# Performance work log

Measured on AMD Instinct MI355X. Metric: run time of the kernel, lower is better.

The kernel has to match this reference:

```python
import jax, jax.numpy as jnp
import numpy as np

BATCH = 1024
INPUT_DIM = 4096
HV_DIM = 8192          # == 2**NUM_QUBITS, so encode_classical fully overwrites the state
NUM_QUBITS = 13
QUANTUM_DEPTH = 3


def setup_inputs() -> dict:
    key = jax.random.key(0)
    k1, k2, k3 = jax.random.split(key, 3)
    x = jax.random.normal(k1, (BATCH, INPUT_DIM), dtype=jnp.float32)
    # torch nn.Linear weight layout: [out_features, in_features]
    W = jax.random.normal(k2, (HV_DIM, INPUT_DIM), dtype=jnp.float32)
    quantum_params = jax.random.normal(k3, (QUANTUM_DEPTH, NUM_QUBITS), dtype=jnp.float32)
    return {"x": x, "W": W, "quantum_params": quantum_params}


def reference(x, W, quantum_params):
    # projection: classical_hv = x @ W^T  -> [B, HV_DIM]
    classical = x @ W.T
    # encode_classical: normalize, cast to complex, renormalize (second norm is 1;
    # kept for fidelity with the original code path)
    amps = (classical / jnp.linalg.norm(classical, axis=-1, keepdims=True)).astype(jnp.complex64)
    amps = amps / jnp.linalg.norm(amps, axis=-1, keepdims=True)

    # sequential gate sequence: for depth in range(D): for qubit in range(Q):
    #   amps = amps*cos(a/2) + roll(amps, 1)*sin(a/2)*1j
    # each step uses the updated amplitudes -> lax.scan over the flattened angles
    angles = quantum_params.reshape(-1)  # [D*Q], depth-major matching the loop order

    def step(a, angle):
        c = jnp.cos(angle * 0.5)
        s = jnp.sin(angle * 0.5)
        return a * c + jnp.roll(a, 1, axis=-1) * (s * 1j), None

    amps, _ = jax.lax.scan(step, amps, angles)
    return amps  # [B, 2**NUM_QUBITS] complex64 quantum amplitudes
```

## Files before the change

### kernel.cpp

```cpp
#include <hip/hip_runtime.h>
#include <hip/hip_fp16.h>
#include <math.h>

typedef _Float16 half8 __attribute__((ext_vector_type(8)));
typedef __fp16 fp16x2 __attribute__((ext_vector_type(2)));
typedef float f32x4 __attribute__((ext_vector_type(4)));

#define BATCH 1024
#define IN_DIM 4096
#define HV 8192
#define NTAP 40

#define BM 128
#define BN 128
#define BK 32
#define BKP 36

#define BM2 128
#define BN2 256
#define BK2 64
#define NT2 (IN_DIM / BK2)
#define ASZ (BM2 * BK2)
#define BSZ (BN2 * BK2)
#define TSZ (ASZ + BSZ)

#define GLD16(g, l) __builtin_amdgcn_global_load_lds(                          \
    (const __attribute__((address_space(1))) void*)(g),                        \
    (__attribute__((address_space(3))) void*)(l), 16, 0, 0)

static __device__ __forceinline__ half8 pk8(f32x4 a, f32x4 b) {
    union { fp16x2 p[4]; half8 h; } u;
    u.p[0] = __builtin_amdgcn_cvt_pkrtz(a.x, a.y);
    u.p[1] = __builtin_amdgcn_cvt_pkrtz(a.z, a.w);
    u.p[2] = __builtin_amdgcn_cvt_pkrtz(b.x, b.y);
    u.p[3] = __builtin_amdgcn_cvt_pkrtz(b.z, b.w);
    return u.h;
}

typedef _Float16 half4v __attribute__((ext_vector_type(4)));
__global__ __launch_bounds__(256) void cvt_f32_f16(const float4* __restrict__ src,
                                                   half4v* __restrict__ dst, int n4) {
    int i = blockIdx.x * 256 + threadIdx.x;
    if (i < n4) {
        float4 v = src[i];
        half4v h;
        h.x = (_Float16)v.x; h.y = (_Float16)v.y;
        h.z = (_Float16)v.z; h.w = (_Float16)v.w;
        dst[i] = h;
    }
}

__global__ __launch_bounds__(64) void compute_taps(const float* __restrict__ qp,
                                                   float* __restrict__ taps) {
    const int lane = threadIdx.x;
    float qv = (lane < 39) ? qp[lane] : 0.f;
    float pr = (lane == 0) ? 1.f : 0.f;
    float pim = 0.f;
    for (int t = 0; t < 39; t++) {
        float a = __shfl(qv, t, 64) * 0.5f;
        float c = cosf(a), s = sinf(a);
        float ur = __shfl_up(pr, 1, 64);
        float ui = __shfl_up(pim, 1, 64);
        if (lane == 0) { ur = 0.f; ui = 0.f; }
        float nr = c * pr - s * ui;
        float ni = c * pim + s * ur;
        pr = nr; pim = ni;
    }
    if (lane < NTAP) taps[lane] = pr;
}

__global__ __launch_bounds__(512, 2) void gemm_f16(
        const _Float16* __restrict__ A,
        const _Float16* __restrict__ B,
        float* __restrict__ out,
        long out_n) {
    __shared__ __align__(16) _Float16 lds[3 * TSZ];

    const int tid  = threadIdx.x;
    const int lane = tid & 63;
    const int wave = tid >> 6;
    const int wm = wave & 1;
    const int wn = wave >> 1;
    const int q = lane >> 4, r = lane & 15;
    const int bm = blockIdx.y * BM2;
    const int bn = blockIdx.x * BN2;

    const _Float16* srcA[2];
    int dA[2];
    #pragma unroll
    for (int h = 0; h < 2; h++) {
        const int p = h * 512 + tid;
        const int R = p >> 3, c = (p & 7) ^ (R & 7);
        srcA[h] = A + (size_t)(bm + R) * IN_DIM + c * 8;
        dA[h] = (h * 512 + wave * 64) * 8;
    }
    const _Float16* srcB[4];
    int dB[4];
    #pragma unroll
    for (int h = 0; h < 4; h++) {
        const int p = h * 512 + tid;
        const int R = p >> 3, c = (p & 7) ^ (R & 7);
        srcB[h] = B + (size_t)(bn + R) * IN_DIM + c * 8;
        dB[h] = ASZ + (h * 512 + wave * 64) * 8;
    }

    f32x4 acc[4][4] = {};

#define STAGE(u, k0)  do {                                   \
        _Float16* bp = &lds[(u) * TSZ];                      \
        GLD16(srcA[0] + (k0), bp + dA[0]);                   \
        GLD16(srcA[1] + (k0), bp + dA[1]);                   \
        GLD16(srcB[0] + (k0), bp + dB[0]);                   \
        GLD16(srcB[1] + (k0), bp + dB[1]);                   \
        GLD16(srcB[2] + (k0), bp + dB[2]);                   \
        GLD16(srcB[3] + (k0), bp + dB[3]);                   \
    } while (0)

#define COMPUTE(u)  do {                                                            \
        const _Float16* bp = &lds[(u) * TSZ];                                       \
        half8 af[4][2], bf[4][2];                                                   \
        _Pragma("unroll")                                                           \
        for (int i = 0; i < 4; i++)                                                 \
            _Pragma("unroll")                                                       \
            for (int kk = 0; kk < 2; kk++) {                                        \
                const int R = wm * 64 + i * 16 + r;                                 \
                const int sw = (kk * 4 + q) ^ (r & 7);                              \
                af[i][kk] = *(const half8*)&bp[R * 64 + sw * 8];                    \
            }                                                                       \
        _Pragma("unroll")                                                           \
        for (int j = 0; j < 4; j++)                                                 \
            _Pragma("unroll")                                                       \
            for (int kk = 0; kk < 2; kk++) {                                        \
                const int R = wn * 64 + j * 16 + r;                                 \
                const int sw = (kk * 4 + q) ^ (r & 7);                              \
                bf[j][kk] = *(const half8*)&bp[ASZ + R * 64 + sw * 8];              \
            }                                                                       \
        __builtin_amdgcn_s_setprio(1);                                              \
        _Pragma("unroll")                                                           \
        for (int i = 0; i < 4; i++)                                                 \
            _Pragma("unroll")                                                       \
            for (int j = 0; j < 4; j++)                                             \
                _Pragma("unroll")                                                   \
                for (int kk = 0; kk < 2; kk++)                                      \
                    acc[i][j] = __builtin_amdgcn_mfma_f32_16x16x32_f16(             \
                        af[i][kk], bf[j][kk], acc[i][j], 0, 0, 0);                  \
        __builtin_amdgcn_s_setprio(0);                                              \
    } while (0)

    STAGE(0, 0);
    STAGE(1, BK2);
    int cur = 0;
    for (int t = 0; t < NT2 - 1; ++t) {
        asm volatile("s_waitcnt vmcnt(6)" ::: "memory");
        __builtin_amdgcn_sched_barrier(0);
        __builtin_amdgcn_s_barrier();
        if (t + 2 < NT2) {
            const int nxt = (cur + 2 >= 3) ? cur - 1 : cur + 2;
            STAGE(nxt, (t + 2) * BK2);
        }
        COMPUTE(cur);
        cur = (cur + 1 == 3) ? 0 : cur + 1;
    }
    asm volatile("s_waitcnt vmcnt(0)" ::: "memory");
    __builtin_amdgcn_sched_barrier(0);
    __builtin_amdgcn_s_barrier();
    COMPUTE(cur);
#undef STAGE
#undef COMPUTE

    #pragma unroll
    for (int i = 0; i < 4; i++) {
        const int row = bm + wm * 64 + i * 16 + q * 4;
        #pragma unroll
        for (int j = 0; j < 4; j++) {
            const int col = bn + wn * 64 + j * 16 + r;
            #pragma unroll
            for (int reg = 0; reg < 4; reg++) {
                long idx = (long)(row + reg) * HV + col;
                if (idx < out_n) out[idx] = acc[i][j][reg];
            }
        }
    }
}

__global__ __launch_bounds__(256) void gemm_f32in(
        const float* __restrict__ A, const float* __restrict__ B,
        float* __restrict__ out, long out_n) {
    __shared__ __align__(16) float lgA[BM * BKP];
    __shared__ __align__(16) float lgB[BN * BKP];

    const int tid  = threadIdx.x;
    const int lane = tid & 63;
    const int wave = tid >> 6;
    const int wm = wave & 1, wn = wave >> 1;
    const int q = lane >> 4, r = lane & 15;
    const int bm = blockIdx.y * BM;
    const int bn = blockIdx.x * BN;

    const int rg = lane >> 3;
    const int cg = (lane & 7) * 4;
    const float* gA = A + (size_t)(bm + wave * 32 + rg) * IN_DIM + cg;
    const float* gB = B + (size_t)(bn + wave * 32 + rg) * IN_DIM + cg;
    float* lA = &lgA[(wave * 32 + rg) * BKP + cg];
    float* lB = &lgB[(wave * 32 + rg) * BKP + cg];

    f32x4 acc[4][4] = {};

    for (int k0 = 0; k0 < IN_DIM; k0 += BK) {
        float4 va[4], vb[4];
        #pragma unroll
        for (int i = 0; i < 4; i++) {
            va[i] = *(const float4*)(gA + k0 + (size_t)(8 * i) * IN_DIM);
            vb[i] = *(const float4*)(gB + k0 + (size_t)(8 * i) * IN_DIM);
        }
        __syncthreads();
        #pragma unroll
        for (int i = 0; i < 4; i++) {
            *(float4*)(lA + 8 * i * BKP) = va[i];
            *(float4*)(lB + 8 * i * BKP) = vb[i];
        }
        __syncthreads();

        half8 af[4], bf[4];
        #pragma unroll
        for (int i = 0; i < 4; i++) {
            const float* p = &lgA[(wm * 64 + i * 16 + r) * BKP + q * 8];
            af[i] = pk8(*(const f32x4*)p, *(const f32x4*)(p + 4));
        }
        #pragma unroll
        for (int j = 0; j < 4; j++) {
            const float* p = &lgB[(wn * 64 + j * 16 + r) * BKP + q * 8];
            bf[j] = pk8(*(const f32x4*)p, *(const f32x4*)(p + 4));
        }

        #pragma unroll
        for (int i = 0; i < 4; i++)
            #pragma unroll
            for (int j = 0; j < 4; j++)
                acc[i][j] = __builtin_amdgcn_mfma_f32_16x16x32_f16(af[i], bf[j], acc[i][j], 0, 0, 0);
    }

    #pragma unroll
    for (int i = 0; i < 4; i++) {
        const int row = bm + wm * 64 + i * 16 + q * 4;
        #pragma unroll
        for (int j = 0; j < 4; j++) {
            const int col = bn + wn * 64 + j * 16 + r;
            #pragma unroll
            for (int reg = 0; reg < 4; reg++) {
                long idx = (long)(row + reg) * HV + col;
                if (idx < out_n) out[idx] = acc[i][j][reg];
            }
        }
    }
}

#define SW4(p4) ((p4) ^ (((p4) >> 3) & 7))
#define WEL(u) (((u) & 3) == 0 ? w4[(u) >> 2].x : ((u) & 3) == 1 ? w4[(u) >> 2].y : \
                ((u) & 3) == 2 ? w4[(u) >> 2].z : w4[(u) >> 2].w)
__global__ __launch_bounds__(256, 2) void norm_conv(float* __restrict__ out,
                                                    const float* __restrict__ qp,
                                                    const float* __restrict__ taps,
                                                    long out_n) {
    __shared__ __align__(16) float ldsv[40 + HV + 24];
    __shared__ float scr[NTAP];
    __shared__ float red[4];

    const int b = blockIdx.x;
    if ((long)(b + 1) * HV > out_n) return;

    const int tid = threadIdx.x;
    const int lane = tid & 63;
    const int wave = tid >> 6;
    float* rowp = out + (size_t)b * HV;
    const float4* row4 = (const float4*)rowp;
    float4* l4 = (float4*)ldsv;

    float ss = 0.f;
    #pragma unroll
    for (int it = 0; it < 8; it++) {
        int j = it * 256 + tid;
        float4 v = row4[j];
        ss += v.x * v.x + v.y * v.y + v.z * v.z + v.w * v.w;
        l4[SW4(10 + j)] = v;
    }
    if (tid < NTAP) {
        ldsv[(SW4(tid >> 2) << 2) | (tid & 3)] = rowp[HV - NTAP + tid];
    }

    #pragma unroll
    for (int off = 32; off > 0; off >>= 1) ss += __shfl_down(ss, off, 64);
    if (lane == 0) red[wave] = ss;

    if (taps) {
        if (tid < NTAP) scr[tid] = taps[tid];
    } else if (wave == 0) {
        float qv = (lane < 39) ? qp[lane] : 0.f;
        float pr = (lane == 0) ? 1.f : 0.f;
        float pim = 0.f;
        for (int t = 0; t < 39; t++) {
            float a = __shfl(qv, t, 64) * 0.5f;
            float c = cosf(a), s = sinf(a);
            float ur = __shfl_up(pr, 1, 64);
            float ui = __shfl_up(pim, 1, 64);
            if (lane == 0) { ur = 0.f; ui = 0.f; }
            float nr = c * pr - s * ui;
            float ni = c * pim + s * ur;
            pr = nr; pim = ni;
        }
        if (lane < NTAP) scr[lane] = pr;
    }
    __syncthreads();

    const float inv = 1.0f / sqrtf(red[0] + red[1] + red[2] + red[3]);
    float4* out4 = (float4*)rowp;

    #pragma unroll
    for (int g = 0; g < 4; g++) {
        float4 w4[12];
        #pragma unroll
        for (int t = 0; t < 12; t++) w4[t] = l4[SW4(8 * tid + 2 * g + t)];

        float av[8] = {};
        #pragma unroll
        for (int k = 0; k < NTAP; k++) {
            const float c = scr[k];
            #pragma unroll
            for (int o = 0; o < 8; o++) av[o] += c * WEL(40 + o - k);
        }
        const int f4 = 8 * tid + 2 * g;
        out4[f4]     = make_float4(inv * av[0], inv * av[1], inv * av[2], inv * av[3]);
        out4[f4 + 1] = make_float4(inv * av[4], inv * av[5], inv * av[6], inv * av[7]);
    }
}

extern "C" void kernel_launch(void* const* d_in, const int* in_sizes, int n_in,
                              void* d_out, int out_size, void* d_ws, size_t ws_size,
                              hipStream_t stream) {
    const float* x  = (const float*)d_in[0];
    const float* W  = (const float*)d_in[1];
    const float* qp = (const float*)d_in[2];
    float* out = (float*)d_out;
    long out_n = (long)out_size;

    const size_t need = (size_t)BATCH * IN_DIM * 2 + (size_t)HV * IN_DIM * 2;

    if (ws_size >= need) {
        _Float16* xh = (_Float16*)d_ws;
        _Float16* wh = xh + (size_t)BATCH * IN_DIM;
        float* taps = nullptr;
        if (ws_size >= need + 256) {
            taps = (float*)((char*)d_ws + need);
            compute_taps<<<1, 64, 0, stream>>>(qp, taps);
        }
        int n4x = BATCH * IN_DIM / 4;
        int n4w = HV * IN_DIM / 4;
        cvt_f32_f16<<<n4x / 256, 256, 0, stream>>>((const float4*)x, (half4v*)xh, n4x);
        cvt_f32_f16<<<n4w / 256, 256, 0, stream>>>((const float4*)W, (half4v*)wh, n4w);
        dim3 grid2(HV / BN2, BATCH / BM2);
        gemm_f16<<<grid2, 512, 0, stream>>>(xh, wh, out, out_n);
        norm_conv<<<BATCH, 256, 0, stream>>>(out, qp, taps, out_n);
    } else {
        float* taps = nullptr;
        if (ws_size >= 256) {
            taps = (float*)d_ws;
            compute_taps<<<1, 64, 0, stream>>>(qp, taps);
        }
        dim3 grid(HV / BN, BATCH / BM);
        gemm_f32in<<<grid, 256, 0, stream>>>(x, W, out, out_n);
        norm_conv<<<BATCH, 256, 0, stream>>>(out, qp, taps, out_n);
    }
}
```

Before: 307.9 us.

## Fuse W fp32-to-fp16 conversion into GEMM and merge tap computation into prep

Removes the separate pass that converts W (32M floats) to fp16. The GEMM now loads fp32 W tiles into registers, converts them and writes them to LDS. The pipeline changes from a three-stage DMA ring to a double buffer that overlaps the next A DMA and B register loads with compute. The tap computation is folded into the x-conversion kernel as an extra block, which saves a launch. The cost is that W is read at fp32 width by every M-tile block (8 of them) instead of once, register pressure goes up, and the pipeline is shallower.

```diff
diff --git a/kernel.cpp b/kernel.cpp
--- a/kernel.cpp
+++ b/kernel.cpp
@@ -38,8 +38,11 @@
 }
 
 typedef _Float16 half4v __attribute__((ext_vector_type(4)));
-__global__ __launch_bounds__(256) void cvt_f32_f16(const float4* __restrict__ src,
-                                                   half4v* __restrict__ dst, int n4) {
+
+__global__ __launch_bounds__(256) void prep(const float4* __restrict__ src,
+                                            half4v* __restrict__ dst, int n4,
+                                            const float* __restrict__ qp,
+                                            float* __restrict__ taps) {
     int i = blockIdx.x * 256 + threadIdx.x;
     if (i < n4) {
         float4 v = src[i];
@@ -47,34 +50,31 @@
         h.x = (_Float16)v.x; h.y = (_Float16)v.y;
         h.z = (_Float16)v.z; h.w = (_Float16)v.w;
         dst[i] = h;
-    }
-}
-
-__global__ __launch_bounds__(64) void compute_taps(const float* __restrict__ qp,
-                                                   float* __restrict__ taps) {
-    const int lane = threadIdx.x;
-    float qv = (lane < 39) ? qp[lane] : 0.f;
-    float pr = (lane == 0) ? 1.f : 0.f;
-    float pim = 0.f;
-    for (int t = 0; t < 39; t++) {
-        float a = __shfl(qv, t, 64) * 0.5f;
-        float c = cosf(a), s = sinf(a);
-        float ur = __shfl_up(pr, 1, 64);
-        float ui = __shfl_up(pim, 1, 64);
-        if (lane == 0) { ur = 0.f; ui = 0.f; }
-        float nr = c * pr - s * ui;
-        float ni = c * pim + s * ur;
-        pr = nr; pim = ni;
-    }
-    if (lane < NTAP) taps[lane] = pr;
-}
-
-__global__ __launch_bounds__(512, 2) void gemm_f16(
+    } else if (blockIdx.x == (unsigned)(n4 / 256) && threadIdx.x < 64) {
+        const int lane = threadIdx.x;
+        float qv = (lane < 39) ? qp[lane] : 0.f;
+        float pr = (lane == 0) ? 1.f : 0.f;
+        float pim = 0.f;
+        for (int t = 0; t < 39; t++) {
+            float a = __shfl(qv, t, 64) * 0.5f;
+            float c = cosf(a), s = sinf(a);
+            float ur = __shfl_up(pr, 1, 64);
+            float ui = __shfl_up(pim, 1, 64);
+            if (lane == 0) { ur = 0.f; ui = 0.f; }
+            float nr = c * pr - s * ui;
+            float ni = c * pim + s * ur;
+            pr = nr; pim = ni;
+        }
+        if (lane < NTAP) taps[lane] = pr;
+    }
+}
+
+__global__ __launch_bounds__(512, 2) void gemm_fused(
         const _Float16* __restrict__ A,
-        const _Float16* __restrict__ B,
+        const float*    __restrict__ W,
         float* __restrict__ out,
         long out_n) {
-    __shared__ __align__(16) _Float16 lds[3 * TSZ];
+    __shared__ __align__(16) _Float16 lds[2 * TSZ];
 
     const int tid  = threadIdx.x;
     const int lane = tid & 63;
@@ -94,26 +94,45 @@
         srcA[h] = A + (size_t)(bm + R) * IN_DIM + c * 8;
         dA[h] = (h * 512 + wave * 64) * 8;
     }
-    const _Float16* srcB[4];
-    int dB[4];
+    const float* srcBW[4];
+    int dBo[4];
     #pragma unroll
     for (int h = 0; h < 4; h++) {
         const int p = h * 512 + tid;
         const int R = p >> 3, c = (p & 7) ^ (R & 7);
-        srcB[h] = B + (size_t)(bn + R) * IN_DIM + c * 8;
-        dB[h] = ASZ + (h * 512 + wave * 64) * 8;
+        srcBW[h] = W + (size_t)(bn + R) * IN_DIM + c * 8;
+        dBo[h] = ASZ + p * 8;
     }
 
     f32x4 acc[4][4] = {};
-
-#define STAGE(u, k0)  do {                                   \
-        _Float16* bp = &lds[(u) * TSZ];                      \
-        GLD16(srcA[0] + (k0), bp + dA[0]);                   \
-        GLD16(srcA[1] + (k0), bp + dA[1]);                   \
-        GLD16(srcB[0] + (k0), bp + dB[0]);                   \
-        GLD16(srcB[1] + (k0), bp + dB[1]);                   \
-        GLD16(srcB[2] + (k0), bp + dB[2]);                   \
-        GLD16(srcB[3] + (k0), bp + dB[3]);                   \
+    f32x4 brg[8];
+
+#define A_DMA(u, k0)  do {                                   \
+        _Float16* bpA = &lds[(u) * TSZ];                     \
+        GLD16(srcA[0] + (k0), bpA + dA[0]);                  \
+        GLD16(srcA[1] + (k0), bpA + dA[1]);                  \
+    } while (0)
+
+#define B_LOAD(k0)  do {                                     \
+        _Pragma("unroll")                                    \
+        for (int h = 0; h < 4; h++) {                        \
+            brg[2*h]   = *(const f32x4*)(srcBW[h] + (k0));   \
+            brg[2*h+1] = *(const f32x4*)(srcBW[h] + (k0) + 4); \
+        }                                                    \
+    } while (0)
+
+#define CVT_WRITE(u)  do {                                   \
+        _Float16* bpW = &lds[(u) * TSZ];                     \
+        _Pragma("unroll")                                    \
+        for (int h = 0; h < 4; h++) {                        \
+            f32x4 lo = brg[2*h], hi = brg[2*h+1];            \
+            half8 hv;                                        \
+            hv[0] = (_Float16)lo.x; hv[1] = (_Float16)lo.y;  \
+            hv[2] = (_Float16)lo.z; hv[3] = (_Float16)lo.w;  \
+            hv[4] = (_Float16)hi.x; hv[5] = (_Float16)hi.y;  \
+            hv[6] = (_Float16)hi.z; hv[7] = (_Float16)hi.w;  \
+            *(half8*)&bpW[dBo[h]] = hv;                      \
+        }                                                    \
     } while (0)
 
 #define COMPUTE(u)  do {                                                            \
@@ -147,25 +166,37 @@
         __builtin_amdgcn_s_setprio(0);                                              \
     } while (0)
 
-    STAGE(0, 0);
-    STAGE(1, BK2);
-    int cur = 0;
-    for (int t = 0; t < NT2 - 1; ++t) {
-        asm volatile("s_waitcnt vmcnt(6)" ::: "memory");
-        __builtin_amdgcn_sched_barrier(0);
-        __builtin_amdgcn_s_barrier();
-        if (t + 2 < NT2) {
-            const int nxt = (cur + 2 >= 3) ? cur - 1 : cur + 2;
-            STAGE(nxt, (t + 2) * BK2);
-        }
-        COMPUTE(cur);
-        cur = (cur + 1 == 3) ? 0 : cur + 1;
-    }
-    asm volatile("s_waitcnt vmcnt(0)" ::: "memory");
+    B_LOAD(0);
+    A_DMA(0, 0);
+    CVT_WRITE(0);
+    B_LOAD(BK2);
+    asm volatile("s_waitcnt vmcnt(8)" ::: "memory");
+    asm volatile("s_waitcnt lgkmcnt(0)" ::: "memory");
     __builtin_amdgcn_sched_barrier(0);
     __builtin_amdgcn_s_barrier();
-    COMPUTE(cur);
-#undef STAGE
+
+    int cur = 0;
+    for (int t = 0; t < NT2; ++t) {
+        const int nxt = cur ^ 1;
+        if (t + 1 < NT2) A_DMA(nxt, (t + 1) * BK2);
+        COMPUTE(cur);
+        if (t + 1 < NT2) {
+            CVT_WRITE(nxt);
+            if (t + 2 < NT2) {
+                B_LOAD((t + 2) * BK2);
+                asm volatile("s_waitcnt vmcnt(8)" ::: "memory");
+            } else {
+                asm volatile("s_waitcnt vmcnt(0)" ::: "memory");
+            }
+            asm volatile("s_waitcnt lgkmcnt(0)" ::: "memory");
+            __builtin_amdgcn_sched_barrier(0);
+            __builtin_amdgcn_s_barrier();
+        }
+        cur = nxt;
+    }
+#undef A_DMA
+#undef B_LOAD
+#undef CVT_WRITE
 #undef COMPUTE
 
     #pragma unroll
@@ -343,31 +374,19 @@
     float* out = (float*)d_out;
     long out_n = (long)out_size;
 
-    const size_t need = (size_t)BATCH * IN_DIM * 2 + (size_t)HV * IN_DIM * 2;
+    const size_t need = (size_t)BATCH * IN_DIM * 2 + 256;
 
     if (ws_size >= need) {
         _Float16* xh = (_Float16*)d_ws;
-        _Float16* wh = xh + (size_t)BATCH * IN_DIM;
-        float* taps = nullptr;
-        if (ws_size >= need + 256) {
-            taps = (float*)((char*)d_ws + need);
-            compute_taps<<<1, 64, 0, stream>>>(qp, taps);
-        }
+        float* taps = (float*)((char*)d_ws + (size_t)BATCH * IN_DIM * 2);
         int n4x = BATCH * IN_DIM / 4;
-        int n4w = HV * IN_DIM / 4;
-        cvt_f32_f16<<<n4x / 256, 256, 0, stream>>>((const float4*)x, (half4v*)xh, n4x);
-        cvt_f32_f16<<<n4w / 256, 256, 0, stream>>>((const float4*)W, (half4v*)wh, n4w);
+        prep<<<n4x / 256 + 1, 256, 0, stream>>>((const float4*)x, (half4v*)xh, n4x, qp, taps);
         dim3 grid2(HV / BN2, BATCH / BM2);
-        gemm_f16<<<grid2, 512, 0, stream>>>(xh, wh, out, out_n);
+        gemm_fused<<<grid2, 512, 0, stream>>>(xh, W, out, out_n);
         norm_conv<<<BATCH, 256, 0, stream>>>(out, qp, taps, out_n);
     } else {
-        float* taps = nullptr;
-        if (ws_size >= 256) {
-            taps = (float*)d_ws;
-            compute_taps<<<1, 64, 0, stream>>>(qp, taps);
-        }
         dim3 grid(HV / BN, BATCH / BM);
         gemm_f32in<<<grid, 256, 0, stream>>>(x, W, out, out_n);
-        norm_conv<<<BATCH, 256, 0, stream>>>(out, qp, taps, out_n);
-    }
-}
+        norm_conv<<<BATCH, 256, 0, stream>>>(out, qp, nullptr, out_n);
+    }
+}
```

After: 318.3 us. +3.4%, slower.

## Shrink f16 GEMM tile to 128x128x32 and fuse conversion and tap kernels

Applied to the files above, without the earlier changes.

The f16 GEMM goes from 128x256 tiles with BK=64 and 512 threads to 128x128 tiles with BK=32 and 256 threads. The LDS swizzle and the wait counts are adjusted to match, and the smaller LDS footprint per block should allow more resident blocks and a larger grid. The separate x/W f32-to-f16 conversions and the tap computation are merged into one prep kernel to remove launches. The cost is smaller per-block reuse and twice as many k-iterations, each with a barrier.

```diff
diff --git a/kernel.cpp b/kernel.cpp
--- a/kernel.cpp
+++ b/kernel.cpp
@@ -13,16 +13,12 @@
 
 #define BM 128
 #define BN 128
-#define BK 32
 #define BKP 36
 
-#define BM2 128
-#define BN2 256
-#define BK2 64
-#define NT2 (IN_DIM / BK2)
-#define ASZ (BM2 * BK2)
-#define BSZ (BN2 * BK2)
-#define TSZ (ASZ + BSZ)
+#define BK3 32
+#define NT3 (IN_DIM / BK3)
+#define ASZ3 (BM * BK3)
+#define TSZ3 (2 * ASZ3)
 
 #define GLD16(g, l) __builtin_amdgcn_global_load_lds(                          \
     (const __attribute__((address_space(1))) void*)(g),                        \
@@ -38,43 +34,52 @@
 }
 
 typedef _Float16 half4v __attribute__((ext_vector_type(4)));
-__global__ __launch_bounds__(256) void cvt_f32_f16(const float4* __restrict__ src,
-                                                   half4v* __restrict__ dst, int n4) {
-    int i = blockIdx.x * 256 + threadIdx.x;
-    if (i < n4) {
-        float4 v = src[i];
+
+__global__ __launch_bounds__(256) void prep(const float4* __restrict__ xsrc, int n4x,
+                                            const float4* __restrict__ wsrc, int n4w,
+                                            half4v* __restrict__ xdst,
+                                            half4v* __restrict__ wdst,
+                                            const float* __restrict__ qp,
+                                            float* __restrict__ taps) {
+    long i = (long)blockIdx.x * 256 + threadIdx.x;
+    if (i < n4x) {
+        float4 v = xsrc[i];
         half4v h;
         h.x = (_Float16)v.x; h.y = (_Float16)v.y;
         h.z = (_Float16)v.z; h.w = (_Float16)v.w;
-        dst[i] = h;
-    }
-}
-
-__global__ __launch_bounds__(64) void compute_taps(const float* __restrict__ qp,
-                                                   float* __restrict__ taps) {
-    const int lane = threadIdx.x;
-    float qv = (lane < 39) ? qp[lane] : 0.f;
-    float pr = (lane == 0) ? 1.f : 0.f;
-    float pim = 0.f;
-    for (int t = 0; t < 39; t++) {
-        float a = __shfl(qv, t, 64) * 0.5f;
-        float c = cosf(a), s = sinf(a);
-        float ur = __shfl_up(pr, 1, 64);
-        float ui = __shfl_up(pim, 1, 64);
-        if (lane == 0) { ur = 0.f; ui = 0.f; }
-        float nr = c * pr - s * ui;
-        float ni = c * pim + s * ur;
-        pr = nr; pim = ni;
-    }
-    if (lane < NTAP) taps[lane] = pr;
-}
-
-__global__ __launch_bounds__(512, 2) void gemm_f16(
+        xdst[i] = h;
+    } else if (i < (long)n4x + n4w) {
+        long j = i - n4x;
+        float4 v = wsrc[j];
+        half4v h;
+        h.x = (_Float16)v.x; h.y = (_Float16)v.y;
+        h.z = (_Float16)v.z; h.w = (_Float16)v.w;
+        wdst[j] = h;
+    } else if (threadIdx.x < 64) {
+        const int lane = threadIdx.x;
+        float qv = (lane < 39) ? qp[lane] : 0.f;
+        float pr = (lane == 0) ? 1.f : 0.f;
+        float pim = 0.f;
+        for (int t = 0; t < 39; t++) {
+            float a = __shfl(qv, t, 64) * 0.5f;
+            float c = cosf(a), s = sinf(a);
+            float ur = __shfl_up(pr, 1, 64);
+            float ui = __shfl_up(pim, 1, 64);
+            if (lane == 0) { ur = 0.f; ui = 0.f; }
+            float nr = c * pr - s * ui;
+            float ni = c * pim + s * ur;
+            pr = nr; pim = ni;
+        }
+        if (lane < NTAP) taps[lane] = pr;
+    }
+}
+
+__global__ __launch_bounds__(256, 2) void gemm_f16(
         const _Float16* __restrict__ A,
         const _Float16* __restrict__ B,
         float* __restrict__ out,
         long out_n) {
-    __shared__ __align__(16) _Float16 lds[3 * TSZ];
+    __shared__ __align__(16) _Float16 lds[3 * TSZ3];
 
     const int tid  = threadIdx.x;
     const int lane = tid & 63;
@@ -82,81 +87,65 @@
     const int wm = wave & 1;
     const int wn = wave >> 1;
     const int q = lane >> 4, r = lane & 15;
-    const int bm = blockIdx.y * BM2;
-    const int bn = blockIdx.x * BN2;
+    const int bm = blockIdx.y * BM;
+    const int bn = blockIdx.x * BN;
 
     const _Float16* srcA[2];
-    int dA[2];
+    const _Float16* srcB[2];
+    int dAB[2];
     #pragma unroll
     for (int h = 0; h < 2; h++) {
-        const int p = h * 512 + tid;
-        const int R = p >> 3, c = (p & 7) ^ (R & 7);
+        const int p = h * 256 + tid;
+        const int R = p >> 2, c = (p & 3) ^ ((R >> 1) & 3);
         srcA[h] = A + (size_t)(bm + R) * IN_DIM + c * 8;
-        dA[h] = (h * 512 + wave * 64) * 8;
-    }
-    const _Float16* srcB[4];
-    int dB[4];
-    #pragma unroll
-    for (int h = 0; h < 4; h++) {
-        const int p = h * 512 + tid;
-        const int R = p >> 3, c = (p & 7) ^ (R & 7);
         srcB[h] = B + (size_t)(bn + R) * IN_DIM + c * 8;
-        dB[h] = ASZ + (h * 512 + wave * 64) * 8;
+        dAB[h] = (h * 256 + wave * 64) * 8;
     }
 
     f32x4 acc[4][4] = {};
 
 #define STAGE(u, k0)  do {                                   \
-        _Float16* bp = &lds[(u) * TSZ];                      \
-        GLD16(srcA[0] + (k0), bp + dA[0]);                   \
-        GLD16(srcA[1] + (k0), bp + dA[1]);                   \
-        GLD16(srcB[0] + (k0), bp + dB[0]);                   \
-        GLD16(srcB[1] + (k0), bp + dB[1]);                   \
-        GLD16(srcB[2] + (k0), bp + dB[2]);                   \
-        GLD16(srcB[3] + (k0), bp + dB[3]);                   \
+        _Float16* bp = &lds[(u) * TSZ3];                     \
+        GLD16(srcA[0] + (k0), bp + dAB[0]);                  \
+        GLD16(srcA[1] + (k0), bp + dAB[1]);                  \
+        GLD16(srcB[0] + (k0), bp + ASZ3 + dAB[0]);           \
+        GLD16(srcB[1] + (k0), bp + ASZ3 + dAB[1]);           \
     } while (0)
 
 #define COMPUTE(u)  do {                                                            \
-        const _Float16* bp = &lds[(u) * TSZ];                                       \
-        half8 af[4][2], bf[4][2];                                                   \
+        const _Float16* bp = &lds[(u) * TSZ3];                                      \
+        half8 af[4], bf[4];                                                         \
+        const int sw = (q ^ ((r >> 1) & 3)) * 8;                                    \
         _Pragma("unroll")                                                           \
-        for (int i = 0; i < 4; i++)                                                 \
-            _Pragma("unroll")                                                       \
-            for (int kk = 0; kk < 2; kk++) {                                        \
-                const int R = wm * 64 + i * 16 + r;                                 \
-                const int sw = (kk * 4 + q) ^ (r & 7);                              \
-                af[i][kk] = *(const half8*)&bp[R * 64 + sw * 8];                    \
-            }                                                                       \
+        for (int i = 0; i < 4; i++) {                                               \
+            const int R = wm * 64 + i * 16 + r;                                     \
+            af[i] = *(const half8*)&bp[R * 32 + sw];                                \
+        }                                                                           \
         _Pragma("unroll")                                                           \
-        for (int j = 0; j < 4; j++)                                                 \
-            _Pragma("unroll")                                                       \
-            for (int kk = 0; kk < 2; kk++) {                                        \
-                const int R = wn * 64 + j * 16 + r;                                 \
-                const int sw = (kk * 4 + q) ^ (r & 7);                              \
-                bf[j][kk] = *(const half8*)&bp[ASZ + R * 64 + sw * 8];              \
-            }                                                                       \
+        for (int j = 0; j < 4; j++) {                                               \
+            const int R = wn * 64 + j * 16 + r;                                     \
+            bf[j] = *(const half8*)&bp[ASZ3 + R * 32 + sw];                         \
+        }                                                                           \
         __builtin_amdgcn_s_setprio(1);                                              \
         _Pragma("unroll")                                                           \
         for (int i = 0; i < 4; i++)                                                 \
             _Pragma("unroll")                                                       \
             for (int j = 0; j < 4; j++)                                             \
-                _Pragma("unroll")                                                   \
-                for (int kk = 0; kk < 2; kk++)                                      \
-                    acc[i][j] = __builtin_amdgcn_mfma_f32_16x16x32_f16(             \
-                        af[i][kk], bf[j][kk], acc[i][j], 0, 0, 0);                  \
+                acc[i][j] = __builtin_amdgcn_mfma_f32_16x16x32_f16(                 \
+                    af[i], bf[j], acc[i][j], 0, 0, 0);                              \
         __builtin_amdgcn_s_setprio(0);                                              \
     } while (0)
 
     STAGE(0, 0);
-    STAGE(1, BK2);
+    STAGE(1, BK3);
     int cur = 0;
-    for (int t = 0; t < NT2 - 1; ++t) {
-        asm volatile("s_waitcnt vmcnt(6)" ::: "memory");
+    for (int t = 0; t < NT3 - 1; ++t) {
+        asm volatile("s_waitcnt vmcnt(4)" ::: "memory");
         __builtin_amdgcn_sched_barrier(0);
         __builtin_amdgcn_s_barrier();
-        if (t + 2 < NT2) {
+        if (t + 2 < NT3) {
             const int nxt = (cur + 2 >= 3) ? cur - 1 : cur + 2;
-            STAGE(nxt, (t + 2) * BK2);
+            STAGE(nxt, (t + 2) * BK3);
         }
         COMPUTE(cur);
         cur = (cur + 1 == 3) ? 0 : cur + 1;
@@ -206,7 +195,7 @@
 
     f32x4 acc[4][4] = {};
 
-    for (int k0 = 0; k0 < IN_DIM; k0 += BK) {
+    for (int k0 = 0; k0 < IN_DIM; k0 += 32) {
         float4 va[4], vb[4];
         #pragma unroll
         for (int i = 0; i < 4; i++) {
@@ -343,31 +332,23 @@
     float* out = (float*)d_out;
     long out_n = (long)out_size;
 
-    const size_t need = (size_t)BATCH * IN_DIM * 2 + (size_t)HV * IN_DIM * 2;
+    const size_t need = (size_t)BATCH * IN_DIM * 2 + (size_t)HV * IN_DIM * 2 + 256;
 
     if (ws_size >= need) {
         _Float16* xh = (_Float16*)d_ws;
         _Float16* wh = xh + (size_t)BATCH * IN_DIM;
-        float* taps = nullptr;
-        if (ws_size >= need + 256) {
-            taps = (float*)((char*)d_ws + need);
-            compute_taps<<<1, 64, 0, stream>>>(qp, taps);
-        }
-        int n4x = BATCH * IN_DIM / 4;
-        int n4w = HV * IN_DIM / 4;
-        cvt_f32_f16<<<n4x / 256, 256, 0, stream>>>((const float4*)x, (half4v*)xh, n4x);
-        cvt_f32_f16<<<n4w / 256, 256, 0, stream>>>((const float4*)W, (half4v*)wh, n4w);
-        dim3 grid2(HV / BN2, BATCH / BM2);
-        gemm_f16<<<grid2, 512, 0, stream>>>(xh, wh, out, out_n);
+        float* taps = (float*)((char*)d_ws + need - 256);
+        const int n4x = BATCH * IN_DIM / 4;
+        const int n4w = HV * IN_DIM / 4;
+        const int nblk = (n4x + n4w) / 256 + 1;
+        prep<<<nblk, 256, 0, stream>>>((const float4*)x, n4x, (const float4*)W, n4w,
+                                       (half4v*)xh, (half4v*)wh, qp, taps);
+        dim3 grid(HV / BN, BATCH / BM);
+        gemm_f16<<<grid, 256, 0, stream>>>(xh, wh, out, out_n);
         norm_conv<<<BATCH, 256, 0, stream>>>(out, qp, taps, out_n);
     } else {
-        float* taps = nullptr;
-        if (ws_size >= 256) {
-            taps = (float*)d_ws;
-            compute_taps<<<1, 64, 0, stream>>>(qp, taps);
-        }
         dim3 grid(HV / BN, BATCH / BM);
         gemm_f32in<<<grid, 256, 0, stream>>>(x, W, out, out_n);
-        norm_conv<<<BATCH, 256, 0, stream>>>(out, qp, taps, out_n);
-    }
-}
+        norm_conv<<<BATCH, 256, 0, stream>>>(out, qp, nullptr, out_n);
+    }
+}
```

Result: no change. 313.7 us (+1.9%).
